# Optimization experiments

Measured on AMD Instinct MI355X. Metric: run time of the kernel, lower is better.

The kernel has to match this reference:

```python
import jax, jax.numpy as jnp
import numpy as np

HEADS = 8
DIM_HEAD = 64
SCALE = DIM_HEAD ** -0.5


def setup_inputs() -> dict:
    key = jax.random.key(0)
    k1, k2, k3 = jax.random.split(key, 3)
    B, N, D = 4, 2048, 512
    inner = HEADS * DIM_HEAD  # 512
    x = jax.random.normal(k1, (B, N, D), dtype=jnp.float32)
    # nn.Linear stores weight [out, in]; y = x @ W.T
    w_qkv = jax.random.normal(k2, (3 * inner, D), dtype=jnp.float32) * (D ** -0.5)
    w_out = jax.random.normal(k3, (D, inner), dtype=jnp.float32) * (inner ** -0.5)
    b_out = jnp.zeros((D,), dtype=jnp.float32)
    return {"x": x, "w_qkv": w_qkv, "w_out": w_out, "b_out": b_out}


def reference(x, w_qkv, w_out, b_out):
    B, N, D = x.shape
    qkv = jnp.einsum('bnd,ed->bne', x, w_qkv)  # [B,N,3*inner]
    q, k, v = jnp.split(qkv, 3, axis=-1)
    def to_heads(t):
        return t.reshape(B, N, HEADS, DIM_HEAD).transpose(0, 2, 1, 3)  # [B,H,N,Dh]
    q, k, v = to_heads(q), to_heads(k), to_heads(v)
    dots = jnp.einsum('bhid,bhjd->bhij', q, k) * SCALE  # [B,H,N,N]
    attn = jax.nn.softmax(dots, axis=-1)
    out = jnp.einsum('bhij,bhjd->bhid', attn, v)  # [B,H,N,Dh]
    out = out.transpose(0, 2, 1, 3).reshape(B, N, HEADS * DIM_HEAD)
    return jnp.einsum('bne,de->bnd', out, w_out) + b_out
```

## Files before the change

### kernel.cpp

```cpp
#include <hip/hip_runtime.h>
#include <hip/hip_bf16.h>
#include <stdint.h>

typedef __bf16 bf16;
typedef __bf16 bf16x8 __attribute__((ext_vector_type(8)));
typedef __bf16 bf16x4 __attribute__((ext_vector_type(4)));
typedef float f32x4 __attribute__((ext_vector_type(4)));

template <int V> struct Int { static constexpr int value = V; };

static __device__ __forceinline__ void gl2lds16(const void* g, void* l) {
  const __attribute__((address_space(1))) void* gp =
      reinterpret_cast<const __attribute__((address_space(1))) void*>(
          reinterpret_cast<uintptr_t>(g));
  __attribute__((address_space(3))) void* lp =
      reinterpret_cast<__attribute__((address_space(3))) void*>(
          static_cast<uint32_t>(reinterpret_cast<uintptr_t>(l)));
  __builtin_amdgcn_global_load_lds(gp, lp, 16, 0, 0);
}

__global__ __launch_bounds__(256) void cvt_f32_bf16(const float* __restrict__ src,
                                                    bf16* __restrict__ dst, int n4) {
  int i = blockIdx.x * blockDim.x + threadIdx.x;
  const int stride = gridDim.x * blockDim.x;
  for (; i < n4; i += stride) {
    const float4 v = reinterpret_cast<const float4*>(src)[i];
    bf16x4 o;
    o[0] = (bf16)v.x; o[1] = (bf16)v.y; o[2] = (bf16)v.z; o[3] = (bf16)v.w;
    reinterpret_cast<bf16x4*>(dst)[i] = o;
  }
}

__global__ __launch_bounds__(256) void qkv_gemm(const bf16* __restrict__ X,
                                                const bf16* __restrict__ W,
                                                bf16* __restrict__ Qb,
                                                bf16* __restrict__ Kb,
                                                bf16* __restrict__ Vt) {
  __shared__ __align__(16) bf16 AshX[8192];
  __shared__ __align__(16) bf16 BshX[8192];
  const int t = threadIdx.x;
  const int lane = t & 63;
  const int w = t >> 6;
  const int fr = lane & 15, fg = lane >> 4;
  const int wr = w >> 1, wc = w & 1;
  const int m0 = blockIdx.x * 128;
  const int n0 = blockIdx.y * 128;
  const int r0 = t >> 2, seg = t & 3;
  const bf16* pA0 = X + (m0 + r0) * 512 + seg * 8;
  const bf16* pA1 = X + (m0 + r0 + 64) * 512 + seg * 8;
  const bf16* pB0 = W + (n0 + r0) * 512 + seg * 8;
  const bf16* pB1 = W + (n0 + r0 + 64) * 512 + seg * 8;
  const bf16* ap = AshX + (wr * 64 + fr) * 32 + fg * 8;
  const bf16* bp = BshX + (wc * 64 + fr) * 32 + fg * 8;

  f32x4 acc[4][4] = {};

  auto stage = [&](auto Bt) {
    constexpr int B = decltype(Bt)::value;
    gl2lds16(pA0, (void*)(AshX + B * 4096 + t * 8));
    gl2lds16(pA1, (void*)(AshX + B * 4096 + 2048 + t * 8));
    gl2lds16(pB0, (void*)(BshX + B * 4096 + t * 8));
    gl2lds16(pB1, (void*)(BshX + B * 4096 + 2048 + t * 8));
    pA0 += 32; pA1 += 32; pB0 += 32; pB1 += 32;
  };
  auto step = [&](auto Bt) {
    constexpr int B = decltype(Bt)::value;
    bf16x8 a[4], b[4];
#pragma unroll
    for (int m = 0; m < 4; ++m) a[m] = *reinterpret_cast<const bf16x8*>(ap + B * 4096 + m * 512);
#pragma unroll
    for (int n = 0; n < 4; ++n) b[n] = *reinterpret_cast<const bf16x8*>(bp + B * 4096 + n * 512);
#pragma unroll
    for (int m = 0; m < 4; ++m)
#pragma unroll
      for (int n = 0; n < 4; ++n)
        acc[m][n] = __builtin_amdgcn_mfma_f32_16x16x32_bf16(a[m], b[n], acc[m][n], 0, 0, 0);
  };

  stage(Int<0>{});
  __syncthreads();
  for (int kt = 0; kt < 16; kt += 2) {
    stage(Int<1>{});
    step(Int<0>{});
    __syncthreads();
    if (kt < 14) stage(Int<0>{});
    step(Int<1>{});
    __syncthreads();
  }

  const int which = n0 >> 9;
#pragma unroll
  for (int n = 0; n < 4; ++n) {
    const int e = n0 + wc * 64 + 16 * n + fr;
    const int h = (e >> 6) & 7;
    const int d = e & 63;
#pragma unroll
    for (int m = 0; m < 4; ++m) {
      const int mbase = m0 + wr * 64 + 16 * m + fg * 4;
      if (which == 2) {
        bf16x4 pk;
#pragma unroll
        for (int r = 0; r < 4; ++r) pk[r] = (bf16)acc[m][n][r];
        const int b = mbase >> 11, tok = mbase & 2047;
        *reinterpret_cast<bf16x4*>(&Vt[((b * 8 + h) * 64 + d) * 2048 + tok]) = pk;
      } else {
        bf16* dst = (which == 0) ? Qb : Kb;
        const float sc = (which == 0) ? (0.125f * 1.44269504088896f) : 1.0f;
#pragma unroll
        for (int r = 0; r < 4; ++r) {
          const int row = mbase + r;
          const int b = row >> 11, tok = row & 2047;
          dst[((b * 8 + h) * 2048 + tok) * 64 + d] = (bf16)(acc[m][n][r] * sc);
        }
      }
    }
  }
}

__global__ __launch_bounds__(256, 2) void attn_fwd(const bf16* __restrict__ Qb,
                                                   const bf16* __restrict__ Kb,
                                                   const bf16* __restrict__ Vt,
                                                   bf16* __restrict__ Ob) {
  __shared__ __align__(16) bf16 sh[16384];
  const int t = threadIdx.x;
  const int lane = t & 63;
  const int w = t >> 6;
  const int fr = lane & 15, fg = lane >> 4;
  const int bh = blockIdx.x;
  const int q0 = blockIdx.y * 128 + 32 * w;

  const bf16* Qrow = Qb + (bh * 2048 + q0 + fr) * 64;
  const bf16x8 qa0 = *reinterpret_cast<const bf16x8*>(Qrow + fg * 8);
  const bf16x8 qa1 = *reinterpret_cast<const bf16x8*>(Qrow + 32 + fg * 8);
  const bf16x8 qb0 = *reinterpret_cast<const bf16x8*>(Qrow + 1024 + fg * 8);
  const bf16x8 qb1 = *reinterpret_cast<const bf16x8*>(Qrow + 1024 + 32 + fg * 8);

  bf16x8 ones;
#pragma unroll
  for (int i = 0; i < 8; ++i) ones[i] = (bf16)1.0f;

  const int c0row = t >> 3, cseg = t & 7;
  const int c1row = c0row + 32;
  const int s0 = (cseg ^ (c0row & 7)) * 8;
  const int s1 = (cseg ^ (c1row & 7)) * 8;
  const int kp0 = 32 * ((c0row >> 4) >> 1) + 8 * ((c0row & 15) >> 2) +
                  4 * ((c0row >> 4) & 1) + (c0row & 3);
  const int kp1 = 32 * ((c1row >> 4) >> 1) + 8 * ((c1row & 15) >> 2) +
                  4 * ((c1row >> 4) & 1) + (c1row & 3);
  const bf16* pK0 = Kb + bh * 131072 + kp0 * 64 + s0;
  const bf16* pK1 = Kb + bh * 131072 + kp1 * 64 + s1;
  const bf16* pV0 = Vt + bh * 131072 + c0row * 2048 + s0;
  const bf16* pV1 = Vt + bh * 131072 + c1row * 2048 + s1;

  const int swz = (fr & 7) << 4;
  const int ko0 = fr * 128 + ((fg * 16) ^ swz);
  const int ko1 = fr * 128 + ((64 + fg * 16) ^ swz);
  const char* shb = reinterpret_cast<const char*>(sh);

  f32x4 oA[4] = {}, oB[4] = {};
  f32x4 lA = {}, lB = {};

  auto stage = [&](auto Bt) {
    constexpr int B = decltype(Bt)::value;
    gl2lds16(pK0, (void*)(sh + B * 4096 + t * 8));
    gl2lds16(pK1, (void*)(sh + B * 4096 + 2048 + t * 8));
    gl2lds16(pV0, (void*)(sh + 8192 + B * 4096 + t * 8));
    gl2lds16(pV1, (void*)(sh + 8192 + B * 4096 + 2048 + t * 8));
    pK0 += 4096; pK1 += 4096; pV0 += 64; pV1 += 64;
  };

  auto compute = [&](auto Bt) {
    constexpr int B = decltype(Bt)::value;
    f32x4 sA[4] = {}, sB[4] = {};
#pragma unroll
    for (int j = 0; j < 4; ++j) {
      const bf16x8 kf0 = *reinterpret_cast<const bf16x8*>(shb + ko0 + (B * 8192 + j * 2048));
      sA[j] = __builtin_amdgcn_mfma_f32_16x16x32_bf16(kf0, qa0, sA[j], 0, 0, 0);
      sB[j] = __builtin_amdgcn_mfma_f32_16x16x32_bf16(kf0, qb0, sB[j], 0, 0, 0);
      const bf16x8 kf1 = *reinterpret_cast<const bf16x8*>(shb + ko1 + (B * 8192 + j * 2048));
      sA[j] = __builtin_amdgcn_mfma_f32_16x16x32_bf16(kf1, qa1, sA[j], 0, 0, 0);
      sB[j] = __builtin_amdgcn_mfma_f32_16x16x32_bf16(kf1, qb1, sB[j], 0, 0, 0);
    }
    bf16x8 pA[2], pB[2];
#pragma unroll
    for (int j = 0; j < 4; ++j)
#pragma unroll
      for (int r = 0; r < 4; ++r) {
        pA[j >> 1][4 * (j & 1) + r] = (bf16)exp2f(sA[j][r]);
        pB[j >> 1][4 * (j & 1) + r] = (bf16)exp2f(sB[j][r]);
      }
    __builtin_amdgcn_s_setprio(1);
#pragma unroll
    for (int ss = 0; ss < 2; ++ss) {
      lA = __builtin_amdgcn_mfma_f32_16x16x32_bf16(ones, pA[ss], lA, 0, 0, 0);
      lB = __builtin_amdgcn_mfma_f32_16x16x32_bf16(ones, pB[ss], lB, 0, 0, 0);
#pragma unroll
      for (int j = 0; j < 4; ++j) {
        const bf16x8 vf = *reinterpret_cast<const bf16x8*>(
            shb + (ss ? ko1 : ko0) + (16384 + B * 8192 + j * 2048));
        oA[j] = __builtin_amdgcn_mfma_f32_16x16x32_bf16(vf, pA[ss], oA[j], 0, 0, 0);
        oB[j] = __builtin_amdgcn_mfma_f32_16x16x32_bf16(vf, pB[ss], oB[j], 0, 0, 0);
      }
    }
    __builtin_amdgcn_s_setprio(0);
  };

  stage(Int<0>{});
  __syncthreads();
  for (int kt = 0; kt < 32; kt += 2) {
    stage(Int<1>{});
    compute(Int<0>{});
    __syncthreads();
    if (kt < 30) stage(Int<0>{});
    compute(Int<1>{});
    __syncthreads();
  }

  const int b = bh >> 3, h = bh & 7;
  const int qA = q0 + fr;
  const float invA = 1.0f / lA[0];
  const float invB = 1.0f / lB[0];
#pragma unroll
  for (int j = 0; j < 4; ++j) {
    bf16x4 o4;
#pragma unroll
    for (int r = 0; r < 4; ++r) o4[r] = (bf16)(oA[j][r] * invA);
    *reinterpret_cast<bf16x4*>(&Ob[(b * 2048 + qA) * 512 + h * 64 + 16 * j + 4 * fg]) = o4;
#pragma unroll
    for (int r = 0; r < 4; ++r) o4[r] = (bf16)(oB[j][r] * invB);
    *reinterpret_cast<bf16x4*>(&Ob[(b * 2048 + qA + 16) * 512 + h * 64 + 16 * j + 4 * fg]) = o4;
  }
}

__global__ __launch_bounds__(256) void out_gemm(const bf16* __restrict__ O,
                                                const bf16* __restrict__ W,
                                                const float* __restrict__ bias,
                                                float* __restrict__ Y) {
  __shared__ __align__(16) bf16 Ash[2][64 * 32];
  __shared__ __align__(16) bf16 Bsh[2][64 * 32];
  const int t = threadIdx.x;
  const int lane = t & 63;
  const int w = t >> 6;
  const int fr = lane & 15, fg = lane >> 4;
  const int m0 = blockIdx.x * 64;
  const int n0 = blockIdx.y * 64;
  const int srow = t >> 2, sseg = t & 3;
  const bf16* gA = O + (m0 + srow) * 512 + sseg * 8;
  const bf16* gB = W + (n0 + srow) * 512 + sseg * 8;

  f32x4 acc[4] = {};
  gl2lds16(gA, &Ash[0][t * 8]);
  gl2lds16(gB, &Bsh[0][t * 8]);
  __syncthreads();
  int cur = 0;
  for (int kt = 0; kt < 16; ++kt) {
    if (kt < 15) {
      gl2lds16(gA + (kt + 1) * 32, &Ash[cur ^ 1][t * 8]);
      gl2lds16(gB + (kt + 1) * 32, &Bsh[cur ^ 1][t * 8]);
    }
    const bf16x8 a = *reinterpret_cast<const bf16x8*>(&Ash[cur][(16 * w + fr) * 32 + fg * 8]);
#pragma unroll
    for (int j = 0; j < 4; ++j) {
      const bf16x8 b = *reinterpret_cast<const bf16x8*>(&Bsh[cur][(16 * j + fr) * 32 + fg * 8]);
      acc[j] = __builtin_amdgcn_mfma_f32_16x16x32_bf16(a, b, acc[j], 0, 0, 0);
    }
    __syncthreads();
    cur ^= 1;
  }
  const int mbase = m0 + 16 * w + fg * 4;
#pragma unroll
  for (int j = 0; j < 4; ++j) {
    const int col = n0 + 16 * j + fr;
    const float bv = bias[col];
#pragma unroll
    for (int r = 0; r < 4; ++r) {
      Y[(mbase + r) * 512 + col] = acc[j][r] + bv;
    }
  }
}

extern "C" void kernel_launch(void* const* d_in, const int* in_sizes, int n_in,
                              void* d_out, int out_size, void* d_ws, size_t ws_size,
                              hipStream_t stream) {
  const float* x = (const float*)d_in[0];
  const float* w_qkv = (const float*)d_in[1];
  const float* w_out = (const float*)d_in[2];
  const float* b_out = (const float*)d_in[3];
  float* y = (float*)d_out;
  char* ws = (char*)d_ws;
  bf16* xb    = (bf16*)(ws);
  bf16* wqkvb = (bf16*)(ws + 8388608);
  bf16* woutb = (bf16*)(ws + 9961472);
  bf16* Qb    = (bf16*)(ws + 10485760);
  bf16* Kb    = (bf16*)(ws + 18874368);
  bf16* Vt    = (bf16*)(ws + 27262976);
  bf16* Ob    = (bf16*)(ws + 35651584);

  hipLaunchKernelGGL(cvt_f32_bf16, dim3(2048), dim3(256), 0, stream, x, xb, 4194304 / 4);
  hipLaunchKernelGGL(cvt_f32_bf16, dim3(768), dim3(256), 0, stream, w_qkv, wqkvb, 786432 / 4);
  hipLaunchKernelGGL(cvt_f32_bf16, dim3(256), dim3(256), 0, stream, w_out, woutb, 262144 / 4);
  hipLaunchKernelGGL(qkv_gemm, dim3(64, 12), dim3(256), 0, stream, xb, wqkvb, Qb, Kb, Vt);
  hipLaunchKernelGGL(attn_fwd, dim3(32, 16), dim3(256), 0, stream, Qb, Kb, Vt, Ob);
  hipLaunchKernelGGL(out_gemm, dim3(128, 8), dim3(256), 0, stream, Ob, woutb, b_out, y);
}
```

Before: 94.73 us.

## Halve attention query tile per wave and enlarge out-projection GEMM tile

The attention kernel now gives each wave 16 query rows instead of 32. That halves the block's query tile to 64, doubles the grid to 1024 blocks, and raises the occupancy hint to 4 blocks per CU. The cost is that each K/V tile loaded into LDS is reused by half as many queries, so global and LDS traffic per FLOP roughly doubles. The output GEMM moves to 128x64 tiles with a 2x2 wave layout and 4x2 MFMA fragments per wave, using double-buffered async LDS loads. This improves register-level reuse and halves its grid.

```diff
diff --git a/kernel.cpp b/kernel.cpp
--- a/kernel.cpp
+++ b/kernel.cpp
@@ -117,7 +117,7 @@
   }
 }
 
-__global__ __launch_bounds__(256, 2) void attn_fwd(const bf16* __restrict__ Qb,
+__global__ __launch_bounds__(256, 4) void attn_fwd(const bf16* __restrict__ Qb,
                                                    const bf16* __restrict__ Kb,
                                                    const bf16* __restrict__ Vt,
                                                    bf16* __restrict__ Ob) {
@@ -127,13 +127,11 @@
   const int w = t >> 6;
   const int fr = lane & 15, fg = lane >> 4;
   const int bh = blockIdx.x;
-  const int q0 = blockIdx.y * 128 + 32 * w;
+  const int q0 = blockIdx.y * 64 + 16 * w;
 
   const bf16* Qrow = Qb + (bh * 2048 + q0 + fr) * 64;
-  const bf16x8 qa0 = *reinterpret_cast<const bf16x8*>(Qrow + fg * 8);
-  const bf16x8 qa1 = *reinterpret_cast<const bf16x8*>(Qrow + 32 + fg * 8);
-  const bf16x8 qb0 = *reinterpret_cast<const bf16x8*>(Qrow + 1024 + fg * 8);
-  const bf16x8 qb1 = *reinterpret_cast<const bf16x8*>(Qrow + 1024 + 32 + fg * 8);
+  const bf16x8 qf0 = *reinterpret_cast<const bf16x8*>(Qrow + fg * 8);
+  const bf16x8 qf1 = *reinterpret_cast<const bf16x8*>(Qrow + 32 + fg * 8);
 
   bf16x8 ones;
 #pragma unroll
@@ -157,8 +155,8 @@
   const int ko1 = fr * 128 + ((64 + fg * 16) ^ swz);
   const char* shb = reinterpret_cast<const char*>(sh);
 
-  f32x4 oA[4] = {}, oB[4] = {};
-  f32x4 lA = {}, lB = {};
+  f32x4 oacc[4] = {};
+  f32x4 lacc = {};
 
   auto stage = [&](auto Bt) {
     constexpr int B = decltype(Bt)::value;
@@ -171,35 +169,30 @@
 
   auto compute = [&](auto Bt) {
     constexpr int B = decltype(Bt)::value;
-    f32x4 sA[4] = {}, sB[4] = {};
+    f32x4 s[4] = {};
 #pragma unroll
     for (int j = 0; j < 4; ++j) {
       const bf16x8 kf0 = *reinterpret_cast<const bf16x8*>(shb + ko0 + (B * 8192 + j * 2048));
-      sA[j] = __builtin_amdgcn_mfma_f32_16x16x32_bf16(kf0, qa0, sA[j], 0, 0, 0);
-      sB[j] = __builtin_amdgcn_mfma_f32_16x16x32_bf16(kf0, qb0, sB[j], 0, 0, 0);
+      s[j] = __builtin_amdgcn_mfma_f32_16x16x32_bf16(kf0, qf0, s[j], 0, 0, 0);
       const bf16x8 kf1 = *reinterpret_cast<const bf16x8*>(shb + ko1 + (B * 8192 + j * 2048));
-      sA[j] = __builtin_amdgcn_mfma_f32_16x16x32_bf16(kf1, qa1, sA[j], 0, 0, 0);
-      sB[j] = __builtin_amdgcn_mfma_f32_16x16x32_bf16(kf1, qb1, sB[j], 0, 0, 0);
+      s[j] = __builtin_amdgcn_mfma_f32_16x16x32_bf16(kf1, qf1, s[j], 0, 0, 0);
     }
-    bf16x8 pA[2], pB[2];
+    bf16x8 pf[2];
 #pragma unroll
     for (int j = 0; j < 4; ++j)
 #pragma unroll
       for (int r = 0; r < 4; ++r) {
-        pA[j >> 1][4 * (j & 1) + r] = (bf16)exp2f(sA[j][r]);
-        pB[j >> 1][4 * (j & 1) + r] = (bf16)exp2f(sB[j][r]);
+        pf[j >> 1][4 * (j & 1) + r] = (bf16)exp2f(s[j][r]);
       }
     __builtin_amdgcn_s_setprio(1);
 #pragma unroll
     for (int ss = 0; ss < 2; ++ss) {
-      lA = __builtin_amdgcn_mfma_f32_16x16x32_bf16(ones, pA[ss], lA, 0, 0, 0);
-      lB = __builtin_amdgcn_mfma_f32_16x16x32_bf16(ones, pB[ss], lB, 0, 0, 0);
+      lacc = __builtin_amdgcn_mfma_f32_16x16x32_bf16(ones, pf[ss], lacc, 0, 0, 0);
 #pragma unroll
       for (int j = 0; j < 4; ++j) {
         const bf16x8 vf = *reinterpret_cast<const bf16x8*>(
             shb + (ss ? ko1 : ko0) + (16384 + B * 8192 + j * 2048));
-        oA[j] = __builtin_amdgcn_mfma_f32_16x16x32_bf16(vf, pA[ss], oA[j], 0, 0, 0);
-        oB[j] = __builtin_amdgcn_mfma_f32_16x16x32_bf16(vf, pB[ss], oB[j], 0, 0, 0);
+        oacc[j] = __builtin_amdgcn_mfma_f32_16x16x32_bf16(vf, pf[ss], oacc[j], 0, 0, 0);
       }
     }
     __builtin_amdgcn_s_setprio(0);
@@ -217,18 +210,14 @@
   }
 
   const int b = bh >> 3, h = bh & 7;
-  const int qA = q0 + fr;
-  const float invA = 1.0f / lA[0];
-  const float invB = 1.0f / lB[0];
+  const int q = q0 + fr;
+  const float inv = 1.0f / lacc[0];
 #pragma unroll
   for (int j = 0; j < 4; ++j) {
     bf16x4 o4;
 #pragma unroll
-    for (int r = 0; r < 4; ++r) o4[r] = (bf16)(oA[j][r] * invA);
-    *reinterpret_cast<bf16x4*>(&Ob[(b * 2048 + qA) * 512 + h * 64 + 16 * j + 4 * fg]) = o4;
-#pragma unroll
-    for (int r = 0; r < 4; ++r) o4[r] = (bf16)(oB[j][r] * invB);
-    *reinterpret_cast<bf16x4*>(&Ob[(b * 2048 + qA + 16) * 512 + h * 64 + 16 * j + 4 * fg]) = o4;
+    for (int r = 0; r < 4; ++r) o4[r] = (bf16)(oacc[j][r] * inv);
+    *reinterpret_cast<bf16x4*>(&Ob[(b * 2048 + q) * 512 + h * 64 + 16 * j + 4 * fg]) = o4;
   }
 }
 
@@ -236,45 +225,67 @@
                                                 const bf16* __restrict__ W,
                                                 const float* __restrict__ bias,
                                                 float* __restrict__ Y) {
-  __shared__ __align__(16) bf16 Ash[2][64 * 32];
-  __shared__ __align__(16) bf16 Bsh[2][64 * 32];
+  __shared__ __align__(16) bf16 Ash[8192];
+  __shared__ __align__(16) bf16 Bsh[4096];
   const int t = threadIdx.x;
   const int lane = t & 63;
   const int w = t >> 6;
   const int fr = lane & 15, fg = lane >> 4;
-  const int m0 = blockIdx.x * 64;
+  const int wr = w >> 1, wc = w & 1;
+  const int m0 = blockIdx.x * 128;
   const int n0 = blockIdx.y * 64;
-  const int srow = t >> 2, sseg = t & 3;
-  const bf16* gA = O + (m0 + srow) * 512 + sseg * 8;
-  const bf16* gB = W + (n0 + srow) * 512 + sseg * 8;
-
-  f32x4 acc[4] = {};
-  gl2lds16(gA, &Ash[0][t * 8]);
-  gl2lds16(gB, &Bsh[0][t * 8]);
+  const int r0 = t >> 2, seg = t & 3;
+  const bf16* pA0 = O + (m0 + r0) * 512 + seg * 8;
+  const bf16* pA1 = O + (m0 + r0 + 64) * 512 + seg * 8;
+  const bf16* pB0 = W + (n0 + r0) * 512 + seg * 8;
+  const bf16* ap = Ash + (wr * 64 + fr) * 32 + fg * 8;
+  const bf16* bp = Bsh + (wc * 32 + fr) * 32 + fg * 8;
+
+  f32x4 acc[4][2] = {};
+
+  auto stage = [&](auto Bt) {
+    constexpr int B = decltype(Bt)::value;
+    gl2lds16(pA0, (void*)(Ash + B * 4096 + t * 8));
+    gl2lds16(pA1, (void*)(Ash + B * 4096 + 2048 + t * 8));
+    gl2lds16(pB0, (void*)(Bsh + B * 2048 + t * 8));
+    pA0 += 32; pA1 += 32; pB0 += 32;
+  };
+  auto step = [&](auto Bt) {
+    constexpr int B = decltype(Bt)::value;
+    bf16x8 a[4], b[2];
+#pragma unroll
+    for (int m = 0; m < 4; ++m) a[m] = *reinterpret_cast<const bf16x8*>(ap + B * 4096 + m * 512);
+#pragma unroll
+    for (int n = 0; n < 2; ++n) b[n] = *reinterpret_cast<const bf16x8*>(bp + B * 2048 + n * 512);
+#pragma unroll
+    for (int m = 0; m < 4; ++m)
+#pragma unroll
+      for (int n = 0; n < 2; ++n)
+        acc[m][n] = __builtin_amdgcn_mfma_f32_16x16x32_bf16(a[m], b[n], acc[m][n], 0, 0, 0);
+  };
+
+  stage(Int<0>{});
   __syncthreads();
-  int cur = 0;
-  for (int kt = 0; kt < 16; ++kt) {
-    if (kt < 15) {
-      gl2lds16(gA + (kt + 1) * 32, &Ash[cur ^ 1][t * 8]);
-      gl2lds16(gB + (kt + 1) * 32, &Bsh[cur ^ 1][t * 8]);
-    }
-    const bf16x8 a = *reinterpret_cast<const bf16x8*>(&Ash[cur][(16 * w + fr) * 32 + fg * 8]);
-#pragma unroll
-    for (int j = 0; j < 4; ++j) {
-      const bf16x8 b = *reinterpret_cast<const bf16x8*>(&Bsh[cur][(16 * j + fr) * 32 + fg * 8]);
-      acc[j] = __builtin_amdgcn_mfma_f32_16x16x32_bf16(a, b, acc[j], 0, 0, 0);
-    }
-    __syncthreads();
-    cur ^= 1;
-  }
-  const int mbase = m0 + 16 * w + fg * 4;
-#pragma unroll
-  for (int j = 0; j < 4; ++j) {
-    const int col = n0 + 16 * j + fr;
+  for (int kt = 0; kt < 16; kt += 2) {
+    stage(Int<1>{});
+    step(Int<0>{});
+    __syncthreads();
+    if (kt < 14) stage(Int<0>{});
+    step(Int<1>{});
+    __syncthreads();
+  }
+
+#pragma unroll
+  for (int n = 0; n < 2; ++n) {
+    const int col = n0 + wc * 32 + 16 * n + fr;
     const float bv = bias[col];
 #pragma unroll
-    for (int r = 0; r < 4; ++r) {
-      Y[(mbase + r) * 512 + col] = acc[j][r] + bv;
+    for (int m = 0; m < 4; ++m) {
+      const int mbase = m0 + wr * 64 + 16 * m + fg * 4;
+#pragma unroll
+      for (int r = 0; r < 4; ++r) {
+        Y[(mbase + r) * 512 + col] = acc[m][n][r] + bv;
+      }
     }
   }
 }
@@ -300,6 +311,6 @@
   hipLaunchKernelGGL(cvt_f32_bf16, dim3(768), dim3(256), 0, stream, w_qkv, wqkvb, 786432 / 4);
   hipLaunchKernelGGL(cvt_f32_bf16, dim3(256), dim3(256), 0, stream, w_out, woutb, 262144 / 4);
   hipLaunchKernelGGL(qkv_gemm, dim3(64, 12), dim3(256), 0, stream, xb, wqkvb, Qb, Kb, Vt);
-  hipLaunchKernelGGL(attn_fwd, dim3(32, 16), dim3(256), 0, stream, Qb, Kb, Vt, Ob);
-  hipLaunchKernelGGL(out_gemm, dim3(128, 8), dim3(256), 0, stream, Ob, woutb, b_out, y);
-}
+  hipLaunchKernelGGL(attn_fwd, dim3(32, 32), dim3(256), 0, stream, Qb, Kb, Vt, Ob);
+  hipLaunchKernelGGL(out_gemm, dim3(64, 8), dim3(256), 0, stream, Ob, woutb, b_out, y);
+}
```

After: 97.46 us. 2.9% more time.
